# Kernel optimization log

Measured on AMD Instinct MI355X. Metric: run time of the kernel, lower is better.

The kernel has to match this reference:

```python
import jax, jax.numpy as jnp
import numpy as np

N = 100000   # nodes
E = 1600000  # edges
D = 128      # input feature dim
H = 128      # hidden dim
C = 40       # output classes


def _gcn_conv(x, W, b, src, dst, norm):
    # PyG GCNConv: h = x @ W; out_i = sum_j (d_i^-1/2 d_j^-1/2) h_j over in-edges,
    # including self-loops, then + bias. norm = deg^-1/2 with self-loop-augmented degree.
    h = x @ W                                    # [N, H]
    coef = norm[src] * norm[dst]                 # [E]
    agg = jax.ops.segment_sum(h[src] * coef[:, None], dst, num_segments=N)
    agg = agg + h * (norm * norm)[:, None]       # self-loop term
    return agg + b


def setup_inputs() -> dict:
    key = jax.random.key(0)
    ks = jax.random.split(key, 12)
    x = jax.random.normal(ks[0], (N, D), dtype=jnp.float32)
    edge_index = jax.random.randint(ks[1], (2, E), 0, N, dtype=jnp.int64)

    def lin(k, fan_in, fan_out):
        s = 1.0 / np.sqrt(fan_in)
        return jax.random.uniform(k, (fan_in, fan_out), jnp.float32, -s, s)

    return {
        "x": x,
        "edge_index": edge_index,
        "W1": lin(ks[2], D, H), "b1": jnp.zeros((H,), jnp.float32),
        "W2": lin(ks[3], H, H), "b2": jnp.zeros((H,), jnp.float32),
        "W3": lin(ks[4], H, H), "b3": jnp.zeros((H,), jnp.float32),
        "Wp1": lin(ks[5], H, H), "bp1": jnp.zeros((H,), jnp.float32),
        "Wp2": lin(ks[6], H, C), "bp2": jnp.zeros((C,), jnp.float32),
    }


def reference(x, edge_index, W1, b1, W2, b2, W3, b3, Wp1, bp1, Wp2, bp2):
    src, dst = edge_index[0], edge_index[1]
    # degree with self-loops (GCNConv adds self-loops by default)
    deg = jax.ops.segment_sum(jnp.ones((E,), jnp.float32), dst, num_segments=N) + 1.0
    norm = jax.lax.rsqrt(deg)                    # deg^-1/2

    h = x
    for W, b in ((W1, b1), (W2, b2), (W3, b3)):
        h = _gcn_conv(h, W, b, src, dst, norm)
        h = jax.nn.relu(h)
        # dropout is a no-op at inference / rate 0

    h = h @ Wp1 + bp1
    h = h @ Wp2 + bp2
    return jax.nn.log_softmax(h, axis=1)
```

## Files before the change

### kernel.cpp

```cpp
#include <hip/hip_runtime.h>
#include <hip/hip_bf16.h>
#include <math.h>


#define DH 128
#define NC 40
#define BN 256
#define MAXNB 512
#define CH 8192
#define ECAP 6144

typedef __attribute__((ext_vector_type(8))) short bf16x8;
typedef __attribute__((ext_vector_type(4))) float f32x4;

__device__ __forceinline__ unsigned short f2bf(float f) {
    unsigned u = __float_as_uint(f);
    unsigned r = (u + 0x7fffu + ((u >> 16) & 1u)) >> 16;
    return (unsigned short)r;
}
__device__ __forceinline__ unsigned pack2(float lo, float hi) {
    return (unsigned)f2bf(lo) | ((unsigned)f2bf(hi) << 16);
}


__global__ __launch_bounds__(256) void bucket_hist(const int* __restrict__ dst, int E,
                                                   unsigned* __restrict__ bcnt) {
    __shared__ unsigned h[MAXNB];
    int tid = threadIdx.x;
    for (int i = tid; i < MAXNB; i += 256) h[i] = 0;
    __syncthreads();
    int e0 = blockIdx.x * CH;
    int e1 = min(e0 + CH, E);
    for (int i = e0 + tid; i < e1; i += 256)
        atomicAdd(&h[dst[i] >> 8], 1u);
    __syncthreads();
    for (int i = tid; i < MAXNB; i += 256)
        if (h[i]) atomicAdd(&bcnt[i], h[i]);
}

__global__ __launch_bounds__(256) void bucket_alloc(const unsigned* __restrict__ bcnt,
                                                    unsigned* __restrict__ bbase,
                                                    unsigned* __restrict__ bpos,
                                                    unsigned* __restrict__ cursor, int NB) {
    int i = blockIdx.x * 256 + threadIdx.x;
    if (i < NB) {
        unsigned c = bcnt[i];
        unsigned o = atomicAdd(cursor, c);
        bbase[i] = o;
        bpos[i] = o;
    }
}

__global__ __launch_bounds__(256) void bucket_scatter(const int* __restrict__ src,
                                                      const int* __restrict__ dst, int E,
                                                      unsigned* __restrict__ bpos,
                                                      unsigned* __restrict__ ebuf) {
    __shared__ unsigned hist[MAXNB];
    __shared__ unsigned lbase[MAXNB];
    __shared__ unsigned gbase[MAXNB];
    __shared__ unsigned cur[MAXNB];
    __shared__ unsigned sorted[CH];
    __shared__ unsigned short sbkt[CH];
    __shared__ unsigned total;

    int tid = threadIdx.x;
    int e0 = blockIdx.x * CH;
    int nE = min(CH, E - e0);

    for (int i = tid; i < MAXNB; i += 256) { hist[i] = 0; cur[i] = 0; }
    if (tid == 0) total = 0;
    __syncthreads();

    for (int i = tid; i < nE; i += 256)
        atomicAdd(&hist[dst[e0 + i] >> 8], 1u);
    __syncthreads();

    for (int i = tid; i < MAXNB; i += 256) {
        unsigned h = hist[i];
        lbase[i] = h ? atomicAdd(&total, h) : 0u;
        gbase[i] = h ? atomicAdd(&bpos[i], h) : 0u;
    }
    __syncthreads();

    for (int i = tid; i < nE; i += 256) {
        int s = src[e0 + i];
        int d = dst[e0 + i];
        unsigned b = (unsigned)d >> 8;
        unsigned r = atomicAdd(&cur[b], 1u);
        unsigned p = lbase[b] + r;
        sorted[p] = ((unsigned)s << 8) | ((unsigned)d & 255u);
        sbkt[p] = (unsigned short)b;
    }
    __syncthreads();

    for (int p = tid; p < nE; p += 256) {
        unsigned b = sbkt[p];
        ebuf[gbase[b] + (p - lbase[b])] = sorted[p];
    }
}

__global__ __launch_bounds__(256) void bucket_csr(const unsigned* __restrict__ ebuf,
                                                  const unsigned* __restrict__ bbase,
                                                  const unsigned* __restrict__ bcnt,
                                                  unsigned* __restrict__ off,
                                                  unsigned* __restrict__ cnt,
                                                  float* __restrict__ nrm,
                                                  int* __restrict__ csr, int N) {
    __shared__ unsigned h[BN];
    __shared__ unsigned nb[BN];
    __shared__ unsigned ncur[BN];
    __shared__ int lcsr[ECAP];
    __shared__ unsigned tot;

    int b = blockIdx.x;
    int tid = threadIdx.x;
    unsigned ebase = bbase[b];
    unsigned ecnt = bcnt[b];

    h[tid] = 0;
    if (tid == 0) tot = 0;
    __syncthreads();

    for (unsigned i = tid; i < ecnt; i += 256)
        atomicAdd(&h[ebuf[ebase + i] & 255u], 1u);
    __syncthreads();

    unsigned myh = h[tid];
    unsigned mybase = myh ? atomicAdd(&tot, myh) : 0u;
    nb[tid] = mybase;
    ncur[tid] = 0;
    int node = b * BN + tid;
    if (node < N) {
        off[node] = ebase + mybase;
        cnt[node] = myh;
        nrm[node] = rsqrtf((float)myh + 1.0f);
    }
    __syncthreads();

    if (ecnt <= ECAP) {
        for (unsigned i = tid; i < ecnt; i += 256) {
            unsigned v = ebuf[ebase + i];
            unsigned nl = v & 255u;
            unsigned r = atomicAdd(&ncur[nl], 1u);
            lcsr[nb[nl] + r] = (int)(v >> 8);
        }
        __syncthreads();
        for (unsigned i = tid; i < ecnt; i += 256)
            csr[ebase + i] = lcsr[i];
    } else {
        for (unsigned i = tid; i < ecnt; i += 256) {
            unsigned v = ebuf[ebase + i];
            unsigned nl = v & 255u;
            unsigned r = atomicAdd(&ncur[nl], 1u);
            csr[ebase + nb[nl] + r] = (int)(v >> 8);
        }
    }
}


__global__ __launch_bounds__(256) void cast_x(const float* __restrict__ x,
                                              unsigned short* __restrict__ xb, int n4) {
    int i = blockIdx.x * 256 + threadIdx.x;
    if (i < n4) {
        float4 v = ((const float4*)x)[i];
        ushort4 o;
        o.x = f2bf(v.x); o.y = f2bf(v.y); o.z = f2bf(v.z); o.w = f2bf(v.w);
        ((ushort4*)xb)[i] = o;
    }
}

__global__ __launch_bounds__(256) void cast_w(const float* __restrict__ W1,
                                              const float* __restrict__ W2,
                                              const float* __restrict__ W3,
                                              unsigned short* __restrict__ Wt) {
    int id = blockIdx.x * 256 + threadIdx.x;
    if (id < 3 * DH * DH) {
        int l = id >> 14, r = id & (DH * DH - 1);
        int k = r >> 7, n = r & 127;
        const float* W = (l == 0) ? W1 : (l == 1) ? W2 : W3;
        Wt[l * DH * DH + n * DH + k] = f2bf(W[k * DH + n]);
    }
}

__global__ __launch_bounds__(256) void fuse_w(const float* __restrict__ Wp1,
                                              const float* __restrict__ bp1,
                                              const float* __restrict__ Wp2,
                                              const float* __restrict__ bp2,
                                              unsigned short* __restrict__ Wft,
                                              float* __restrict__ bfh) {
    int o = blockIdx.x * 256 + threadIdx.x;
    if (o < 48 * DH) {
        int c = o >> 7, k = o & 127;
        float acc = 0.f;
        if (c < NC)
            for (int j = 0; j < DH; ++j) acc += Wp1[k * DH + j] * Wp2[j * NC + c];
        Wft[c * DH + k] = f2bf(acc);
    } else if (o < 48 * DH + 48) {
        int c = o - 48 * DH;
        float acc = 0.f;
        if (c < NC) {
            acc = bp2[c];
            for (int j = 0; j < DH; ++j) acc += bp1[j] * Wp2[j * NC + c];
        }
        bfh[c] = acc;
    }
}


__global__ __launch_bounds__(256) void gemm_mfma(const unsigned short* __restrict__ Xb,
                                                 const unsigned short* __restrict__ Wt,
                                                 const float* __restrict__ nrm,
                                                 unsigned short* __restrict__ outb,
                                                 int nrows) {
    const int tid = threadIdx.x;
    const int wave = tid >> 6;
    const int lane = tid & 63;
    const int m = lane & 15;
    const int quad = lane >> 4;
    const int rbase = blockIdx.x * 128 + wave * 32;

    f32x4 acc[2][8];
#pragma unroll
    for (int rt = 0; rt < 2; ++rt)
#pragma unroll
        for (int ct = 0; ct < 8; ++ct) acc[rt][ct] = (f32x4){0.f, 0.f, 0.f, 0.f};

#pragma unroll
    for (int kt = 0; kt < 4; ++kt) {
        const int kof = kt * 32 + quad * 8;
        bf16x8 a[2], b[8];
#pragma unroll
        for (int rt = 0; rt < 2; ++rt) {
            int r = rbase + rt * 16 + m;
            r = (r < nrows) ? r : (nrows - 1);
            a[rt] = *(const bf16x8*)(Xb + (size_t)r * DH + kof);
        }
#pragma unroll
        for (int ct = 0; ct < 8; ++ct)
            b[ct] = *(const bf16x8*)(Wt + (ct * 16 + m) * DH + kof);
#pragma unroll
        for (int rt = 0; rt < 2; ++rt)
#pragma unroll
            for (int ct = 0; ct < 8; ++ct)
                acc[rt][ct] = __builtin_amdgcn_mfma_f32_16x16x32_bf16(a[rt], b[ct], acc[rt][ct], 0, 0, 0);
    }

#pragma unroll
    for (int rt = 0; rt < 2; ++rt)
#pragma unroll
        for (int reg = 0; reg < 4; ++reg) {
            int r = rbase + rt * 16 + quad * 4 + reg;
            if (r < nrows) {
                float s = nrm[r];
#pragma unroll
                for (int ct = 0; ct < 8; ++ct)
                    outb[(size_t)r * DH + ct * 16 + m] = f2bf(acc[rt][ct][reg] * s);
            }
        }
}


__device__ __forceinline__ void bf8_add(float* acc, uint4 v) {
    acc[0] += __uint_as_float(v.x << 16);
    acc[1] += __uint_as_float(v.x & 0xffff0000u);
    acc[2] += __uint_as_float(v.y << 16);
    acc[3] += __uint_as_float(v.y & 0xffff0000u);
    acc[4] += __uint_as_float(v.z << 16);
    acc[5] += __uint_as_float(v.z & 0xffff0000u);
    acc[6] += __uint_as_float(v.w << 16);
    acc[7] += __uint_as_float(v.w & 0xffff0000u);
}

__global__ __launch_bounds__(256) void aggregate(const uint4* __restrict__ Abf,
                                                 const int* __restrict__ csr,
                                                 const unsigned* __restrict__ off,
                                                 const unsigned* __restrict__ cnt,
                                                 const float* __restrict__ nrm,
                                                 const float* __restrict__ bias,
                                                 unsigned short* __restrict__ Bb, int N) {
    int node = blockIdx.x * 16 + (threadIdx.x >> 4);
    int lane = threadIdx.x & 15;
    if (node >= N) return;

    float acc[8];
    {
        uint4 v = Abf[(size_t)node * 16 + lane];
        acc[0] = __uint_as_float(v.x << 16);
        acc[1] = __uint_as_float(v.x & 0xffff0000u);
        acc[2] = __uint_as_float(v.y << 16);
        acc[3] = __uint_as_float(v.y & 0xffff0000u);
        acc[4] = __uint_as_float(v.z << 16);
        acc[5] = __uint_as_float(v.z & 0xffff0000u);
        acc[6] = __uint_as_float(v.w << 16);
        acc[7] = __uint_as_float(v.w & 0xffff0000u);
    }
    unsigned o = off[node];
    unsigned d = cnt[node];

    unsigned e = 0;
    for (; e + 4 <= d; e += 4) {
        int s0 = csr[o + e + 0];
        int s1 = csr[o + e + 1];
        int s2 = csr[o + e + 2];
        int s3 = csr[o + e + 3];
        uint4 v0 = Abf[(size_t)s0 * 16 + lane];
        uint4 v1 = Abf[(size_t)s1 * 16 + lane];
        uint4 v2 = Abf[(size_t)s2 * 16 + lane];
        uint4 v3 = Abf[(size_t)s3 * 16 + lane];
        bf8_add(acc, v0);
        bf8_add(acc, v1);
        bf8_add(acc, v2);
        bf8_add(acc, v3);
    }
    for (; e < d; ++e) {
        int s = csr[o + e];
        uint4 v = Abf[(size_t)s * 16 + lane];
        bf8_add(acc, v);
    }

    float nm = nrm[node];
    float4 b0 = *(const float4*)(bias + lane * 8);
    float4 b1 = *(const float4*)(bias + lane * 8 + 4);
    float r0 = fmaxf(acc[0] * nm + b0.x, 0.f);
    float r1 = fmaxf(acc[1] * nm + b0.y, 0.f);
    float r2 = fmaxf(acc[2] * nm + b0.z, 0.f);
    float r3 = fmaxf(acc[3] * nm + b0.w, 0.f);
    float r4 = fmaxf(acc[4] * nm + b1.x, 0.f);
    float r5 = fmaxf(acc[5] * nm + b1.y, 0.f);
    float r6 = fmaxf(acc[6] * nm + b1.z, 0.f);
    float r7 = fmaxf(acc[7] * nm + b1.w, 0.f);
    uint4 ov;
    ov.x = pack2(r0, r1);
    ov.y = pack2(r2, r3);
    ov.z = pack2(r4, r5);
    ov.w = pack2(r6, r7);
    ((uint4*)Bb)[(size_t)node * 16 + lane] = ov;
}


__global__ __launch_bounds__(256) void final_mfma(const unsigned short* __restrict__ Xb,
                                                  const unsigned short* __restrict__ Wft,
                                                  const float* __restrict__ bfh,
                                                  float* __restrict__ out, int nrows) {
    const int tid = threadIdx.x;
    const int wave = tid >> 6;
    const int lane = tid & 63;
    const int m = lane & 15;
    const int quad = lane >> 4;
    const int rbase = blockIdx.x * 64 + wave * 16;

    f32x4 acc[3];
#pragma unroll
    for (int ct = 0; ct < 3; ++ct) acc[ct] = (f32x4){0.f, 0.f, 0.f, 0.f};

#pragma unroll
    for (int kt = 0; kt < 4; ++kt) {
        const int kof = kt * 32 + quad * 8;
        int r = rbase + m;
        r = (r < nrows) ? r : (nrows - 1);
        bf16x8 a = *(const bf16x8*)(Xb + (size_t)r * DH + kof);
#pragma unroll
        for (int ct = 0; ct < 3; ++ct) {
            bf16x8 b = *(const bf16x8*)(Wft + (ct * 16 + m) * DH + kof);
            acc[ct] = __builtin_amdgcn_mfma_f32_16x16x32_bf16(a, b, acc[ct], 0, 0, 0);
        }
    }

    float bias0 = bfh[m];
    float bias1 = bfh[16 + m];
    float bias2 = bfh[32 + m];

#pragma unroll
    for (int reg = 0; reg < 4; ++reg) {
        float v0 = acc[0][reg] + bias0;
        float v1 = acc[1][reg] + bias1;
        float v2 = (m < 8) ? (acc[2][reg] + bias2) : -1e30f;
        float mx = fmaxf(fmaxf(v0, v1), v2);
#pragma unroll
        for (int dlt = 1; dlt < 16; dlt <<= 1) mx = fmaxf(mx, __shfl_xor(mx, dlt));
        float s = __expf(v0 - mx) + __expf(v1 - mx) + ((m < 8) ? __expf(v2 - mx) : 0.f);
#pragma unroll
        for (int dlt = 1; dlt < 16; dlt <<= 1) s += __shfl_xor(s, dlt);
        float ls = mx + __logf(s);
        int r = rbase + quad * 4 + reg;
        if (r < nrows) {
            out[(size_t)r * NC + m] = v0 - ls;
            out[(size_t)r * NC + 16 + m] = v1 - ls;
            if (m < 8) out[(size_t)r * NC + 32 + m] = v2 - ls;
        }
    }
}


extern "C" void kernel_launch(void* const* d_in, const int* in_sizes, int n_in,
                              void* d_out, int out_size, void* d_ws, size_t ws_size,
                              hipStream_t stream) {
    const float* x   = (const float*)d_in[0];
    const int*   ei  = (const int*)d_in[1];
    const float* W1  = (const float*)d_in[2];
    const float* b1  = (const float*)d_in[3];
    const float* W2  = (const float*)d_in[4];
    const float* b2  = (const float*)d_in[5];
    const float* W3  = (const float*)d_in[6];
    const float* b3  = (const float*)d_in[7];
    const float* Wp1 = (const float*)d_in[8];
    const float* bp1 = (const float*)d_in[9];
    const float* Wp2 = (const float*)d_in[10];
    const float* bp2 = (const float*)d_in[11];
    float* out = (float*)d_out;

    const int N = in_sizes[0] / DH;
    const int E = in_sizes[1] / 2;
    const int* src = ei;
    const int* dst = ei + E;
    const int NB = (N + BN - 1) / BN;

    char* w = (char*)d_ws;
    unsigned short* xb  = (unsigned short*)w; w += (size_t)N * DH * 2;
    unsigned short* Ab  = (unsigned short*)w; w += (size_t)N * DH * 2;
    unsigned short* Bb  = (unsigned short*)w; w += (size_t)N * DH * 2;
    int*      csr    = (int*)w;      w += (size_t)E * 4;
    unsigned* ebuf   = (unsigned*)w; w += (size_t)E * 4;
    unsigned* bcnt   = (unsigned*)w; w += MAXNB * 4;
    unsigned* cursor = (unsigned*)w; w += 16;
    unsigned* bbase  = (unsigned*)w; w += MAXNB * 4;
    unsigned* bpos   = (unsigned*)w; w += MAXNB * 4;
    unsigned* off    = (unsigned*)w; w += (size_t)N * 4;
    unsigned* cnt    = (unsigned*)w; w += (size_t)N * 4;
    float*    nrm    = (float*)w;    w += (size_t)N * 4;
    unsigned short* Wt  = (unsigned short*)w; w += 3 * DH * DH * 2;
    unsigned short* Wft = (unsigned short*)w; w += 48 * DH * 2;
    float*    bfh    = (float*)w;    w += 64 * 4;

    const int gC = (E + CH - 1) / CH;

    hipMemsetAsync(bcnt, 0, MAXNB * 4 + 16, stream);
    bucket_hist   <<<gC, 256, 0, stream>>>(dst, E, bcnt);
    bucket_alloc  <<<(NB + 255) / 256, 256, 0, stream>>>(bcnt, bbase, bpos, cursor, NB);
    bucket_scatter<<<gC, 256, 0, stream>>>(src, dst, E, bpos, ebuf);
    bucket_csr    <<<NB, 256, 0, stream>>>(ebuf, bbase, bcnt, off, cnt, nrm, csr, N);

    cast_x<<<((N * DH / 4) + 255) / 256, 256, 0, stream>>>(x, xb, N * DH / 4);
    cast_w<<<(3 * DH * DH + 255) / 256, 256, 0, stream>>>(W1, W2, W3, Wt);
    fuse_w<<<(48 * DH + 48 + 255) / 256, 256, 0, stream>>>(Wp1, bp1, Wp2, bp2, Wft, bfh);

    const int gG = (N + 127) / 128;
    const int gA = (N + 15) / 16;

    gemm_mfma<<<gG, 256, 0, stream>>>(xb, Wt,              nrm, Ab, N);
    aggregate<<<gA, 256, 0, stream>>>((const uint4*)Ab, csr, off, cnt, nrm, b1, Bb, N);
    gemm_mfma<<<gG, 256, 0, stream>>>(Bb, Wt + DH * DH,     nrm, Ab, N);
    aggregate<<<gA, 256, 0, stream>>>((const uint4*)Ab, csr, off, cnt, nrm, b2, Bb, N);
    gemm_mfma<<<gG, 256, 0, stream>>>(Bb, Wt + 2 * DH * DH, nrm, Ab, N);
    aggregate<<<gA, 256, 0, stream>>>((const uint4*)Ab, csr, off, cnt, nrm, b3, Bb, N);

    final_mfma<<<(N + 63) / 64, 256, 0, stream>>>(Bb, Wft, bfh, out, N);
}
```

Before: 461.3 us.

## Fuse x cast into first GEMM, merge weight prep, split aggregation by column halves

The separate fp32-to-bf16 cast of x is removed; the first GEMM now reads fp32 rows and packs them to bf16 in registers. The two weight-prep kernels are merged into one launch. Aggregation is split into two column halves via a second grid dimension, with each thread gathering 8 bytes and an 8-way unrolled edge loop for more memory-level parallelism. The split doubles CSR index reads and per-node metadata loads, and halves the gather width per edge.

```diff
diff --git a/kernel.cpp b/kernel.cpp
--- a/kernel.cpp
+++ b/kernel.cpp
@@ -158,45 +158,31 @@
 }
 
 
-__global__ __launch_bounds__(256) void cast_x(const float* __restrict__ x,
-                                              unsigned short* __restrict__ xb, int n4) {
-    int i = blockIdx.x * 256 + threadIdx.x;
-    if (i < n4) {
-        float4 v = ((const float4*)x)[i];
-        ushort4 o;
-        o.x = f2bf(v.x); o.y = f2bf(v.y); o.z = f2bf(v.z); o.w = f2bf(v.w);
-        ((ushort4*)xb)[i] = o;
-    }
-}
-
-__global__ __launch_bounds__(256) void cast_w(const float* __restrict__ W1,
+__global__ __launch_bounds__(256) void prep_w(const float* __restrict__ W1,
                                               const float* __restrict__ W2,
                                               const float* __restrict__ W3,
-                                              unsigned short* __restrict__ Wt) {
+                                              const float* __restrict__ Wp1,
+                                              const float* __restrict__ bp1,
+                                              const float* __restrict__ Wp2,
+                                              const float* __restrict__ bp2,
+                                              unsigned short* __restrict__ Wt,
+                                              unsigned short* __restrict__ Wft,
+                                              float* __restrict__ bfh) {
     int id = blockIdx.x * 256 + threadIdx.x;
     if (id < 3 * DH * DH) {
         int l = id >> 14, r = id & (DH * DH - 1);
         int k = r >> 7, n = r & 127;
         const float* W = (l == 0) ? W1 : (l == 1) ? W2 : W3;
         Wt[l * DH * DH + n * DH + k] = f2bf(W[k * DH + n]);
-    }
-}
-
-__global__ __launch_bounds__(256) void fuse_w(const float* __restrict__ Wp1,
-                                              const float* __restrict__ bp1,
-                                              const float* __restrict__ Wp2,
-                                              const float* __restrict__ bp2,
-                                              unsigned short* __restrict__ Wft,
-                                              float* __restrict__ bfh) {
-    int o = blockIdx.x * 256 + threadIdx.x;
-    if (o < 48 * DH) {
+    } else if (id < 3 * DH * DH + 48 * DH) {
+        int o = id - 3 * DH * DH;
         int c = o >> 7, k = o & 127;
         float acc = 0.f;
         if (c < NC)
             for (int j = 0; j < DH; ++j) acc += Wp1[k * DH + j] * Wp2[j * NC + c];
         Wft[c * DH + k] = f2bf(acc);
-    } else if (o < 48 * DH + 48) {
-        int c = o - 48 * DH;
+    } else if (id < 3 * DH * DH + 48 * DH + 48) {
+        int c = id - 3 * DH * DH - 48 * DH;
         float acc = 0.f;
         if (c < NC) {
             acc = bp2[c];
@@ -260,18 +246,77 @@
 }
 
 
-__device__ __forceinline__ void bf8_add(float* acc, uint4 v) {
+__global__ __launch_bounds__(256) void gemm_mfma_f32(const float* __restrict__ X,
+                                                     const unsigned short* __restrict__ Wt,
+                                                     const float* __restrict__ nrm,
+                                                     unsigned short* __restrict__ outb,
+                                                     int nrows) {
+    const int tid = threadIdx.x;
+    const int wave = tid >> 6;
+    const int lane = tid & 63;
+    const int m = lane & 15;
+    const int quad = lane >> 4;
+    const int rbase = blockIdx.x * 128 + wave * 32;
+
+    union U8 { bf16x8 v; unsigned u[4]; };
+
+    f32x4 acc[2][8];
+#pragma unroll
+    for (int rt = 0; rt < 2; ++rt)
+#pragma unroll
+        for (int ct = 0; ct < 8; ++ct) acc[rt][ct] = (f32x4){0.f, 0.f, 0.f, 0.f};
+
+#pragma unroll
+    for (int kt = 0; kt < 4; ++kt) {
+        const int kof = kt * 32 + quad * 8;
+        bf16x8 a[2], b[8];
+#pragma unroll
+        for (int rt = 0; rt < 2; ++rt) {
+            int r = rbase + rt * 16 + m;
+            r = (r < nrows) ? r : (nrows - 1);
+            const float* p = X + (size_t)r * DH + kof;
+            float4 u0 = *(const float4*)p;
+            float4 u1 = *(const float4*)(p + 4);
+            U8 t;
+            t.u[0] = pack2(u0.x, u0.y);
+            t.u[1] = pack2(u0.z, u0.w);
+            t.u[2] = pack2(u1.x, u1.y);
+            t.u[3] = pack2(u1.z, u1.w);
+            a[rt] = t.v;
+        }
+#pragma unroll
+        for (int ct = 0; ct < 8; ++ct)
+            b[ct] = *(const bf16x8*)(Wt + (ct * 16 + m) * DH + kof);
+#pragma unroll
+        for (int rt = 0; rt < 2; ++rt)
+#pragma unroll
+            for (int ct = 0; ct < 8; ++ct)
+                acc[rt][ct] = __builtin_amdgcn_mfma_f32_16x16x32_bf16(a[rt], b[ct], acc[rt][ct], 0, 0, 0);
+    }
+
+#pragma unroll
+    for (int rt = 0; rt < 2; ++rt)
+#pragma unroll
+        for (int reg = 0; reg < 4; ++reg) {
+            int r = rbase + rt * 16 + quad * 4 + reg;
+            if (r < nrows) {
+                float s = nrm[r];
+#pragma unroll
+                for (int ct = 0; ct < 8; ++ct)
+                    outb[(size_t)r * DH + ct * 16 + m] = f2bf(acc[rt][ct][reg] * s);
+            }
+        }
+}
+
+
+__device__ __forceinline__ void bf4_add(float* acc, uint2 v) {
     acc[0] += __uint_as_float(v.x << 16);
     acc[1] += __uint_as_float(v.x & 0xffff0000u);
     acc[2] += __uint_as_float(v.y << 16);
     acc[3] += __uint_as_float(v.y & 0xffff0000u);
-    acc[4] += __uint_as_float(v.z << 16);
-    acc[5] += __uint_as_float(v.z & 0xffff0000u);
-    acc[6] += __uint_as_float(v.w << 16);
-    acc[7] += __uint_as_float(v.w & 0xffff0000u);
-}
-
-__global__ __launch_bounds__(256) void aggregate(const uint4* __restrict__ Abf,
+}
+
+__global__ __launch_bounds__(256) void aggregate(const uint2* __restrict__ Abf,
                                                  const int* __restrict__ csr,
                                                  const unsigned* __restrict__ off,
                                                  const unsigned* __restrict__ cnt,
@@ -280,61 +325,59 @@
                                                  unsigned short* __restrict__ Bb, int N) {
     int node = blockIdx.x * 16 + (threadIdx.x >> 4);
     int lane = threadIdx.x & 15;
+    int half = blockIdx.y;
     if (node >= N) return;
 
-    float acc[8];
+    const int cidx = half * 16 + lane;
+
+    float acc[4];
     {
-        uint4 v = Abf[(size_t)node * 16 + lane];
+        uint2 v = Abf[(size_t)node * 32 + cidx];
         acc[0] = __uint_as_float(v.x << 16);
         acc[1] = __uint_as_float(v.x & 0xffff0000u);
         acc[2] = __uint_as_float(v.y << 16);
         acc[3] = __uint_as_float(v.y & 0xffff0000u);
-        acc[4] = __uint_as_float(v.z << 16);
-        acc[5] = __uint_as_float(v.z & 0xffff0000u);
-        acc[6] = __uint_as_float(v.w << 16);
-        acc[7] = __uint_as_float(v.w & 0xffff0000u);
     }
     unsigned o = off[node];
     unsigned d = cnt[node];
 
     unsigned e = 0;
-    for (; e + 4 <= d; e += 4) {
+    for (; e + 8 <= d; e += 8) {
         int s0 = csr[o + e + 0];
         int s1 = csr[o + e + 1];
         int s2 = csr[o + e + 2];
         int s3 = csr[o + e + 3];
-        uint4 v0 = Abf[(size_t)s0 * 16 + lane];
-        uint4 v1 = Abf[(size_t)s1 * 16 + lane];
-        uint4 v2 = Abf[(size_t)s2 * 16 + lane];
-        uint4 v3 = Abf[(size_t)s3 * 16 + lane];
-        bf8_add(acc, v0);
-        bf8_add(acc, v1);
-        bf8_add(acc, v2);
-        bf8_add(acc, v3);
+        int s4 = csr[o + e + 4];
+        int s5 = csr[o + e + 5];
+        int s6 = csr[o + e + 6];
+        int s7 = csr[o + e + 7];
+        uint2 v0 = Abf[(size_t)s0 * 32 + cidx];
+        uint2 v1 = Abf[(size_t)s1 * 32 + cidx];
+        uint2 v2 = Abf[(size_t)s2 * 32 + cidx];
+        uint2 v3 = Abf[(size_t)s3 * 32 + cidx];
+        uint2 v4 = Abf[(size_t)s4 * 32 + cidx];
+        uint2 v5 = Abf[(size_t)s5 * 32 + cidx];
+        uint2 v6 = Abf[(size_t)s6 * 32 + cidx];
+        uint2 v7 = Abf[(size_t)s7 * 32 + cidx];
+        bf4_add(acc, v0); bf4_add(acc, v1); bf4_add(acc, v2); bf4_add(acc, v3);
+        bf4_add(acc, v4); bf4_add(acc, v5); bf4_add(acc, v6); bf4_add(acc, v7);
     }
     for (; e < d; ++e) {
         int s = csr[o + e];
-        uint4 v = Abf[(size_t)s * 16 + lane];
-        bf8_add(acc, v);
+        uint2 v = Abf[(size_t)s * 32 + cidx];
+        bf4_add(acc, v);
     }
 
     float nm = nrm[node];
-    float4 b0 = *(const float4*)(bias + lane * 8);
-    float4 b1 = *(const float4*)(bias + lane * 8 + 4);
-    float r0 = fmaxf(acc[0] * nm + b0.x, 0.f);
-    float r1 = fmaxf(acc[1] * nm + b0.y, 0.f);
-    float r2 = fmaxf(acc[2] * nm + b0.z, 0.f);
-    float r3 = fmaxf(acc[3] * nm + b0.w, 0.f);
-    float r4 = fmaxf(acc[4] * nm + b1.x, 0.f);
-    float r5 = fmaxf(acc[5] * nm + b1.y, 0.f);
-    float r6 = fmaxf(acc[6] * nm + b1.z, 0.f);
-    float r7 = fmaxf(acc[7] * nm + b1.w, 0.f);
-    uint4 ov;
+    float4 b4 = *(const float4*)(bias + cidx * 4);
+    float r0 = fmaxf(acc[0] * nm + b4.x, 0.f);
+    float r1 = fmaxf(acc[1] * nm + b4.y, 0.f);
+    float r2 = fmaxf(acc[2] * nm + b4.z, 0.f);
+    float r3 = fmaxf(acc[3] * nm + b4.w, 0.f);
+    uint2 ov;
     ov.x = pack2(r0, r1);
     ov.y = pack2(r2, r3);
-    ov.z = pack2(r4, r5);
-    ov.w = pack2(r6, r7);
-    ((uint4*)Bb)[(size_t)node * 16 + lane] = ov;
+    ((uint2*)Bb)[(size_t)node * 32 + cidx] = ov;
 }
 
 
@@ -416,7 +459,6 @@
     const int NB = (N + BN - 1) / BN;
 
     char* w = (char*)d_ws;
-    unsigned short* xb  = (unsigned short*)w; w += (size_t)N * DH * 2;
     unsigned short* Ab  = (unsigned short*)w; w += (size_t)N * DH * 2;
     unsigned short* Bb  = (unsigned short*)w; w += (size_t)N * DH * 2;
     int*      csr    = (int*)w;      w += (size_t)E * 4;
@@ -439,20 +481,18 @@
     bucket_alloc  <<<(NB + 255) / 256, 256, 0, stream>>>(bcnt, bbase, bpos, cursor, NB);
     bucket_scatter<<<gC, 256, 0, stream>>>(src, dst, E, bpos, ebuf);
     bucket_csr    <<<NB, 256, 0, stream>>>(ebuf, bbase, bcnt, off, cnt, nrm, csr, N);
-
-    cast_x<<<((N * DH / 4) + 255) / 256, 256, 0, stream>>>(x, xb, N * DH / 4);
-    cast_w<<<(3 * DH * DH + 255) / 256, 256, 0, stream>>>(W1, W2, W3, Wt);
-    fuse_w<<<(48 * DH + 48 + 255) / 256, 256, 0, stream>>>(Wp1, bp1, Wp2, bp2, Wft, bfh);
+    prep_w<<<(3 * DH * DH + 48 * DH + 48 + 255) / 256, 256, 0, stream>>>(
+        W1, W2, W3, Wp1, bp1, Wp2, bp2, Wt, Wft, bfh);
 
     const int gG = (N + 127) / 128;
-    const int gA = (N + 15) / 16;
-
-    gemm_mfma<<<gG, 256, 0, stream>>>(xb, Wt,              nrm, Ab, N);
-    aggregate<<<gA, 256, 0, stream>>>((const uint4*)Ab, csr, off, cnt, nrm, b1, Bb, N);
+    const dim3 gA((N + 15) / 16, 2);
+
+    gemm_mfma_f32<<<gG, 256, 0, stream>>>(x, Wt, nrm, Ab, N);
+    aggregate<<<gA, 256, 0, stream>>>((const uint2*)Ab, csr, off, cnt, nrm, b1, Bb, N);
     gemm_mfma<<<gG, 256, 0, stream>>>(Bb, Wt + DH * DH,     nrm, Ab, N);
-    aggregate<<<gA, 256, 0, stream>>>((const uint4*)Ab, csr, off, cnt, nrm, b2, Bb, N);
+    aggregate<<<gA, 256, 0, stream>>>((const uint2*)Ab, csr, off, cnt, nrm, b2, Bb, N);
     gemm_mfma<<<gG, 256, 0, stream>>>(Bb, Wt + 2 * DH * DH, nrm, Ab, N);
-    aggregate<<<gA, 256, 0, stream>>>((const uint4*)Ab, csr, off, cnt, nrm, b3, Bb, N);
+    aggregate<<<gA, 256, 0, stream>>>((const uint2*)Ab, csr, off, cnt, nrm, b3, Bb, N);
 
     final_mfma<<<(N + 63) / 64, 256, 0, stream>>>(Bb, Wft, bfh, out, N);
 }
```

New measurement: 464.5 us. Within noise of the previous version (+0.7%).

## Fuse aggregation with next-layer GEMM and head; cast x inside first GEMM

Applied to the files above, without the earlier changes.

Each aggregation kernel now stages its 16 aggregated rows in shared memory and immediately multiplies them by the next layer's weights (or the fused head plus log-softmax) using MFMA. This removes the bf16 round-trip of intermediate activations through global memory and several launches. The separate x-cast kernel is also dropped, with the first GEMM reading fp32 x and packing it to bf16 on the fly. The weight prep kernels are merged into one. The cost is that each fused block does a small 16-row GEMM that re-reads the weights from global memory per block, and the head kernel uses only one wave for its matmul.

```diff
diff --git a/kernel.cpp b/kernel.cpp
--- a/kernel.cpp
+++ b/kernel.cpp
@@ -9,6 +9,7 @@
 #define MAXNB 512
 #define CH 8192
 #define ECAP 6144
+#define SP 136
 
 typedef __attribute__((ext_vector_type(8))) short bf16x8;
 typedef __attribute__((ext_vector_type(4))) float f32x4;
@@ -158,45 +159,31 @@
 }
 
 
-__global__ __launch_bounds__(256) void cast_x(const float* __restrict__ x,
-                                              unsigned short* __restrict__ xb, int n4) {
-    int i = blockIdx.x * 256 + threadIdx.x;
-    if (i < n4) {
-        float4 v = ((const float4*)x)[i];
-        ushort4 o;
-        o.x = f2bf(v.x); o.y = f2bf(v.y); o.z = f2bf(v.z); o.w = f2bf(v.w);
-        ((ushort4*)xb)[i] = o;
-    }
-}
-
-__global__ __launch_bounds__(256) void cast_w(const float* __restrict__ W1,
+__global__ __launch_bounds__(256) void prep_w(const float* __restrict__ W1,
                                               const float* __restrict__ W2,
                                               const float* __restrict__ W3,
-                                              unsigned short* __restrict__ Wt) {
+                                              const float* __restrict__ Wp1,
+                                              const float* __restrict__ bp1,
+                                              const float* __restrict__ Wp2,
+                                              const float* __restrict__ bp2,
+                                              unsigned short* __restrict__ Wt,
+                                              unsigned short* __restrict__ Wft,
+                                              float* __restrict__ bfh) {
     int id = blockIdx.x * 256 + threadIdx.x;
     if (id < 3 * DH * DH) {
         int l = id >> 14, r = id & (DH * DH - 1);
         int k = r >> 7, n = r & 127;
         const float* W = (l == 0) ? W1 : (l == 1) ? W2 : W3;
         Wt[l * DH * DH + n * DH + k] = f2bf(W[k * DH + n]);
-    }
-}
-
-__global__ __launch_bounds__(256) void fuse_w(const float* __restrict__ Wp1,
-                                              const float* __restrict__ bp1,
-                                              const float* __restrict__ Wp2,
-                                              const float* __restrict__ bp2,
-                                              unsigned short* __restrict__ Wft,
-                                              float* __restrict__ bfh) {
-    int o = blockIdx.x * 256 + threadIdx.x;
-    if (o < 48 * DH) {
+    } else if (id < 3 * DH * DH + 48 * DH) {
+        int o = id - 3 * DH * DH;
         int c = o >> 7, k = o & 127;
         float acc = 0.f;
         if (c < NC)
             for (int j = 0; j < DH; ++j) acc += Wp1[k * DH + j] * Wp2[j * NC + c];
         Wft[c * DH + k] = f2bf(acc);
-    } else if (o < 48 * DH + 48) {
-        int c = o - 48 * DH;
+    } else if (id < 3 * DH * DH + 48 * DH + 48) {
+        int c = id - 3 * DH * DH - 48 * DH;
         float acc = 0.f;
         if (c < NC) {
             acc = bp2[c];
@@ -207,11 +194,11 @@
 }
 
 
-__global__ __launch_bounds__(256) void gemm_mfma(const unsigned short* __restrict__ Xb,
-                                                 const unsigned short* __restrict__ Wt,
-                                                 const float* __restrict__ nrm,
-                                                 unsigned short* __restrict__ outb,
-                                                 int nrows) {
+__global__ __launch_bounds__(256) void gemm_mfma_f32(const float* __restrict__ X,
+                                                     const unsigned short* __restrict__ Wt,
+                                                     const float* __restrict__ nrm,
+                                                     unsigned short* __restrict__ outb,
+                                                     int nrows) {
     const int tid = threadIdx.x;
     const int wave = tid >> 6;
     const int lane = tid & 63;
@@ -219,6 +206,8 @@
     const int quad = lane >> 4;
     const int rbase = blockIdx.x * 128 + wave * 32;
 
+    union U8 { bf16x8 v; unsigned u[4]; };
+
     f32x4 acc[2][8];
 #pragma unroll
     for (int rt = 0; rt < 2; ++rt)
@@ -233,7 +222,15 @@
         for (int rt = 0; rt < 2; ++rt) {
             int r = rbase + rt * 16 + m;
             r = (r < nrows) ? r : (nrows - 1);
-            a[rt] = *(const bf16x8*)(Xb + (size_t)r * DH + kof);
+            const float* p = X + (size_t)r * DH + kof;
+            float4 u0 = *(const float4*)p;
+            float4 u1 = *(const float4*)(p + 4);
+            U8 t;
+            t.u[0] = pack2(u0.x, u0.y);
+            t.u[1] = pack2(u0.z, u0.w);
+            t.u[2] = pack2(u1.x, u1.y);
+            t.u[3] = pack2(u1.z, u1.w);
+            a[rt] = t.v;
         }
 #pragma unroll
         for (int ct = 0; ct < 8; ++ct)
@@ -271,94 +268,142 @@
     acc[7] += __uint_as_float(v.w & 0xffff0000u);
 }
 
-__global__ __launch_bounds__(256) void aggregate(const uint4* __restrict__ Abf,
-                                                 const int* __restrict__ csr,
-                                                 const unsigned* __restrict__ off,
-                                                 const unsigned* __restrict__ cnt,
-                                                 const float* __restrict__ nrm,
-                                                 const float* __restrict__ bias,
-                                                 unsigned short* __restrict__ Bb, int N) {
-    int node = blockIdx.x * 16 + (threadIdx.x >> 4);
-    int lane = threadIdx.x & 15;
-    if (node >= N) return;
-
-    float acc[8];
-    {
-        uint4 v = Abf[(size_t)node * 16 + lane];
-        acc[0] = __uint_as_float(v.x << 16);
-        acc[1] = __uint_as_float(v.x & 0xffff0000u);
-        acc[2] = __uint_as_float(v.y << 16);
-        acc[3] = __uint_as_float(v.y & 0xffff0000u);
-        acc[4] = __uint_as_float(v.z << 16);
-        acc[5] = __uint_as_float(v.z & 0xffff0000u);
-        acc[6] = __uint_as_float(v.w << 16);
-        acc[7] = __uint_as_float(v.w & 0xffff0000u);
-    }
-    unsigned o = off[node];
-    unsigned d = cnt[node];
-
-    unsigned e = 0;
-    for (; e + 4 <= d; e += 4) {
-        int s0 = csr[o + e + 0];
-        int s1 = csr[o + e + 1];
-        int s2 = csr[o + e + 2];
-        int s3 = csr[o + e + 3];
-        uint4 v0 = Abf[(size_t)s0 * 16 + lane];
-        uint4 v1 = Abf[(size_t)s1 * 16 + lane];
-        uint4 v2 = Abf[(size_t)s2 * 16 + lane];
-        uint4 v3 = Abf[(size_t)s3 * 16 + lane];
-        bf8_add(acc, v0);
-        bf8_add(acc, v1);
-        bf8_add(acc, v2);
-        bf8_add(acc, v3);
-    }
-    for (; e < d; ++e) {
-        int s = csr[o + e];
-        uint4 v = Abf[(size_t)s * 16 + lane];
-        bf8_add(acc, v);
-    }
-
-    float nm = nrm[node];
-    float4 b0 = *(const float4*)(bias + lane * 8);
-    float4 b1 = *(const float4*)(bias + lane * 8 + 4);
-    float r0 = fmaxf(acc[0] * nm + b0.x, 0.f);
-    float r1 = fmaxf(acc[1] * nm + b0.y, 0.f);
-    float r2 = fmaxf(acc[2] * nm + b0.z, 0.f);
-    float r3 = fmaxf(acc[3] * nm + b0.w, 0.f);
-    float r4 = fmaxf(acc[4] * nm + b1.x, 0.f);
-    float r5 = fmaxf(acc[5] * nm + b1.y, 0.f);
-    float r6 = fmaxf(acc[6] * nm + b1.z, 0.f);
-    float r7 = fmaxf(acc[7] * nm + b1.w, 0.f);
-    uint4 ov;
-    ov.x = pack2(r0, r1);
-    ov.y = pack2(r2, r3);
-    ov.z = pack2(r4, r5);
-    ov.w = pack2(r6, r7);
-    ((uint4*)Bb)[(size_t)node * 16 + lane] = ov;
-}
-
-
-__global__ __launch_bounds__(256) void final_mfma(const unsigned short* __restrict__ Xb,
-                                                  const unsigned short* __restrict__ Wft,
-                                                  const float* __restrict__ bfh,
-                                                  float* __restrict__ out, int nrows) {
+__device__ __forceinline__ void gather_phase(const uint4* __restrict__ Abf,
+                                             const int* __restrict__ csr,
+                                             const unsigned* __restrict__ off,
+                                             const unsigned* __restrict__ cnt,
+                                             const float* __restrict__ nrm,
+                                             const float* __restrict__ bias,
+                                             unsigned short (*sA)[SP], int N) {
+    const int tid = threadIdx.x;
+    const int g = tid >> 4;
+    const int lane = tid & 15;
+    const int node = blockIdx.x * 16 + g;
+    if (node < N) {
+        float acc[8];
+        {
+            uint4 v = Abf[(size_t)node * 16 + lane];
+            acc[0] = __uint_as_float(v.x << 16);
+            acc[1] = __uint_as_float(v.x & 0xffff0000u);
+            acc[2] = __uint_as_float(v.y << 16);
+            acc[3] = __uint_as_float(v.y & 0xffff0000u);
+            acc[4] = __uint_as_float(v.z << 16);
+            acc[5] = __uint_as_float(v.z & 0xffff0000u);
+            acc[6] = __uint_as_float(v.w << 16);
+            acc[7] = __uint_as_float(v.w & 0xffff0000u);
+        }
+        unsigned o = off[node];
+        unsigned d = cnt[node];
+
+        unsigned e = 0;
+        for (; e + 4 <= d; e += 4) {
+            int s0 = csr[o + e + 0];
+            int s1 = csr[o + e + 1];
+            int s2 = csr[o + e + 2];
+            int s3 = csr[o + e + 3];
+            uint4 v0 = Abf[(size_t)s0 * 16 + lane];
+            uint4 v1 = Abf[(size_t)s1 * 16 + lane];
+            uint4 v2 = Abf[(size_t)s2 * 16 + lane];
+            uint4 v3 = Abf[(size_t)s3 * 16 + lane];
+            bf8_add(acc, v0);
+            bf8_add(acc, v1);
+            bf8_add(acc, v2);
+            bf8_add(acc, v3);
+        }
+        for (; e < d; ++e) {
+            int s = csr[o + e];
+            uint4 v = Abf[(size_t)s * 16 + lane];
+            bf8_add(acc, v);
+        }
+
+        float nm = nrm[node];
+        float4 b0 = *(const float4*)(bias + lane * 8);
+        float4 b1 = *(const float4*)(bias + lane * 8 + 4);
+        unsigned short* p = &sA[g][lane * 8];
+        p[0] = f2bf(fmaxf(acc[0] * nm + b0.x, 0.f));
+        p[1] = f2bf(fmaxf(acc[1] * nm + b0.y, 0.f));
+        p[2] = f2bf(fmaxf(acc[2] * nm + b0.z, 0.f));
+        p[3] = f2bf(fmaxf(acc[3] * nm + b0.w, 0.f));
+        p[4] = f2bf(fmaxf(acc[4] * nm + b1.x, 0.f));
+        p[5] = f2bf(fmaxf(acc[5] * nm + b1.y, 0.f));
+        p[6] = f2bf(fmaxf(acc[6] * nm + b1.z, 0.f));
+        p[7] = f2bf(fmaxf(acc[7] * nm + b1.w, 0.f));
+    }
+    __syncthreads();
+}
+
+
+__global__ __launch_bounds__(256) void agg_gemm(const uint4* __restrict__ Abf,
+                                                const int* __restrict__ csr,
+                                                const unsigned* __restrict__ off,
+                                                const unsigned* __restrict__ cnt,
+                                                const float* __restrict__ nrm,
+                                                const float* __restrict__ bias,
+                                                const unsigned short* __restrict__ Wt,
+                                                unsigned short* __restrict__ outb, int N) {
+    __shared__ unsigned short sA[16][SP];
+    gather_phase(Abf, csr, off, cnt, nrm, bias, sA, N);
+
     const int tid = threadIdx.x;
     const int wave = tid >> 6;
-    const int lane = tid & 63;
-    const int m = lane & 15;
-    const int quad = lane >> 4;
-    const int rbase = blockIdx.x * 64 + wave * 16;
-
-    f32x4 acc[3];
-#pragma unroll
-    for (int ct = 0; ct < 3; ++ct) acc[ct] = (f32x4){0.f, 0.f, 0.f, 0.f};
+    const int l64 = tid & 63;
+    const int m = l64 & 15;
+    const int quad = l64 >> 4;
+
+    f32x4 acc[2];
+    acc[0] = (f32x4){0.f, 0.f, 0.f, 0.f};
+    acc[1] = (f32x4){0.f, 0.f, 0.f, 0.f};
 
 #pragma unroll
     for (int kt = 0; kt < 4; ++kt) {
         const int kof = kt * 32 + quad * 8;
-        int r = rbase + m;
-        r = (r < nrows) ? r : (nrows - 1);
-        bf16x8 a = *(const bf16x8*)(Xb + (size_t)r * DH + kof);
+        bf16x8 a = *(const bf16x8*)&sA[m][kof];
+#pragma unroll
+        for (int c2 = 0; c2 < 2; ++c2) {
+            const int ct = wave * 2 + c2;
+            bf16x8 b = *(const bf16x8*)(Wt + (ct * 16 + m) * DH + kof);
+            acc[c2] = __builtin_amdgcn_mfma_f32_16x16x32_bf16(a, b, acc[c2], 0, 0, 0);
+        }
+    }
+
+#pragma unroll
+    for (int reg = 0; reg < 4; ++reg) {
+        int r = blockIdx.x * 16 + quad * 4 + reg;
+        if (r < N) {
+            float s = nrm[r];
+#pragma unroll
+            for (int c2 = 0; c2 < 2; ++c2)
+                outb[(size_t)r * DH + (wave * 2 + c2) * 16 + m] = f2bf(acc[c2][reg] * s);
+        }
+    }
+}
+
+
+__global__ __launch_bounds__(256) void agg_head(const uint4* __restrict__ Abf,
+                                                const int* __restrict__ csr,
+                                                const unsigned* __restrict__ off,
+                                                const unsigned* __restrict__ cnt,
+                                                const float* __restrict__ nrm,
+                                                const float* __restrict__ bias,
+                                                const unsigned short* __restrict__ Wft,
+                                                const float* __restrict__ bfh,
+                                                float* __restrict__ out, int N) {
+    __shared__ unsigned short sA[16][SP];
+    gather_phase(Abf, csr, off, cnt, nrm, bias, sA, N);
+
+    const int tid = threadIdx.x;
+    if (tid >= 64) return;
+    const int m = tid & 15;
+    const int quad = tid >> 4;
+
+    f32x4 acc[3];
+#pragma unroll
+    for (int ct = 0; ct < 3; ++ct) acc[ct] = (f32x4){0.f, 0.f, 0.f, 0.f};
+
+#pragma unroll
+    for (int kt = 0; kt < 4; ++kt) {
+        const int kof = kt * 32 + quad * 8;
+        bf16x8 a = *(const bf16x8*)&sA[m][kof];
 #pragma unroll
         for (int ct = 0; ct < 3; ++ct) {
             bf16x8 b = *(const bf16x8*)(Wft + (ct * 16 + m) * DH + kof);
@@ -382,8 +427,8 @@
 #pragma unroll
         for (int dlt = 1; dlt < 16; dlt <<= 1) s += __shfl_xor(s, dlt);
         float ls = mx + __logf(s);
-        int r = rbase + quad * 4 + reg;
-        if (r < nrows) {
+        int r = blockIdx.x * 16 + quad * 4 + reg;
+        if (r < N) {
             out[(size_t)r * NC + m] = v0 - ls;
             out[(size_t)r * NC + 16 + m] = v1 - ls;
             if (m < 8) out[(size_t)r * NC + 32 + m] = v2 - ls;
@@ -416,7 +461,6 @@
     const int NB = (N + BN - 1) / BN;
 
     char* w = (char*)d_ws;
-    unsigned short* xb  = (unsigned short*)w; w += (size_t)N * DH * 2;
     unsigned short* Ab  = (unsigned short*)w; w += (size_t)N * DH * 2;
     unsigned short* Bb  = (unsigned short*)w; w += (size_t)N * DH * 2;
     int*      csr    = (int*)w;      w += (size_t)E * 4;
@@ -439,20 +483,17 @@
     bucket_alloc  <<<(NB + 255) / 256, 256, 0, stream>>>(bcnt, bbase, bpos, cursor, NB);
     bucket_scatter<<<gC, 256, 0, stream>>>(src, dst, E, bpos, ebuf);
     bucket_csr    <<<NB, 256, 0, stream>>>(ebuf, bbase, bcnt, off, cnt, nrm, csr, N);
-
-    cast_x<<<((N * DH / 4) + 255) / 256, 256, 0, stream>>>(x, xb, N * DH / 4);
-    cast_w<<<(3 * DH * DH + 255) / 256, 256, 0, stream>>>(W1, W2, W3, Wt);
-    fuse_w<<<(48 * DH + 48 + 255) / 256, 256, 0, stream>>>(Wp1, bp1, Wp2, bp2, Wft, bfh);
+    prep_w<<<(3 * DH * DH + 48 * DH + 48 + 255) / 256, 256, 0, stream>>>(
+        W1, W2, W3, Wp1, bp1, Wp2, bp2, Wt, Wft, bfh);
 
     const int gG = (N + 127) / 128;
-    const int gA = (N + 15) / 16;
-
-    gemm_mfma<<<gG, 256, 0, stream>>>(xb, Wt,              nrm, Ab, N);
-    aggregate<<<gA, 256, 0, stream>>>((const uint4*)Ab, csr, off, cnt, nrm, b1, Bb, N);
-    gemm_mfma<<<gG, 256, 0, stream>>>(Bb, Wt + DH * DH,     nrm, Ab, N);
-    aggregate<<<gA, 256, 0, stream>>>((const uint4*)Ab, csr, off, cnt, nrm, b2, Bb, N);
-    gemm_mfma<<<gG, 256, 0, stream>>>(Bb, Wt + 2 * DH * DH, nrm, Ab, N);
-    aggregate<<<gA, 256, 0, stream>>>((const uint4*)Ab, csr, off, cnt, nrm, b3, Bb, N);
-
-    final_mfma<<<(N + 63) / 64, 256, 0, stream>>>(Bb, Wft, bfh, out, N);
-}
+    const int gF = (N + 15) / 16;
+
+    gemm_mfma_f32<<<gG, 256, 0, stream>>>(x, Wt, nrm, Ab, N);
+    agg_gemm<<<gF, 256, 0, stream>>>((const uint4*)Ab, csr, off, cnt, nrm, b1,
+                                     Wt + DH * DH, Bb, N);
+    agg_gemm<<<gF, 256, 0, stream>>>((const uint4*)Bb, csr, off, cnt, nrm, b2,
+                                     Wt + 2 * DH * DH, Ab, N);
+    agg_head<<<gF, 256, 0, stream>>>((const uint4*)Ab, csr, off, cnt, nrm, b3,
+                                     Wft, bfh, out, N);
+}
```

Result: faster. 418.0 us (-9.4%).
